# Performance work log

Hardware: AMD Instinct MI355X
Metric: run time of the kernel (lower is better)

Reference implementation:

```python
import jax, jax.numpy as jnp
import numpy as np

R = 0.4          # ball radius
K = 32           # max_neighbors
S = 512          # cluster_num
BN_EPS = 1e-5


def fps(data, npoint):
    """Furthest point sampling. data: [B,N,C] -> idx [B,npoint] int32.
    Deterministic start at index 0 (original uses randint)."""
    B, N, C = data.shape

    def step(carry, _):
        dist, far = carry
        cent = jnp.take_along_axis(data, far[:, None, None], axis=1)  # [B,1,C]
        d = jnp.sum((data - cent) ** 2, -1)                           # [B,N]
        dist = jnp.minimum(dist, d)
        new_far = jnp.argmax(dist, -1).astype(jnp.int32)
        return (dist, new_far), far

    dist0 = jnp.full((B, N), 1e10, data.dtype)
    far0 = jnp.zeros((B,), jnp.int32)
    _, idxs = jax.lax.scan(step, (dist0, far0), None, length=npoint)
    return idxs.T  # [B,npoint]


def gather_points(data, idx):
    """data [B,N,C], idx [B,S] -> [B,S,C]"""
    return jnp.take_along_axis(data, idx[..., None], axis=1)


def gather_groups(data, idx):
    """data [B,N,C], idx [B,S,K] -> [B,S,K,C]"""
    B, N, C = data.shape
    _, Sq, Kq = idx.shape
    flat = jnp.take_along_axis(data, idx.reshape(B, Sq * Kq)[..., None], axis=1)
    return flat.reshape(B, Sq, Kq, C)


def square_dist(a, b):
    """a [B,N,C], b [B,M,C] -> [B,N,M]"""
    return (-2.0 * jnp.einsum('bnc,bmc->bnm', a, b)
            + jnp.sum(a ** 2, -1)[:, :, None]
            + jnp.sum(b ** 2, -1)[:, None, :])


def knn_query(data, query, max_neighbors, r):
    """Ball query: indices of up to max_neighbors points within r, padded with
    the first valid index. data [B,N,C], query [B,S,C] -> [B,S,K] int32."""
    B, N, _ = data.shape
    d = square_dist(query, data)                              # [B,S,N]
    idx = jnp.where(d <= r * r, jnp.arange(N, dtype=jnp.int32)[None, None, :], N)
    idx = jnp.sort(idx, axis=-1)[:, :, :max_neighbors]        # ascending, N = invalid
    first = idx[:, :, :1]
    return jnp.where(idx == N, first, idx)


def mlp_layer(x, w, b, g, be):
    """1x1 Conv2d + BatchNorm2d (training-mode batch stats) + ReLU.
    x [B,S,K,Cin], w [Cout,Cin] -> [B,S,K,Cout]"""
    y = jnp.einsum('bskc,oc->bsko', x, w) + b
    m = jnp.mean(y, axis=(0, 1, 2))
    v = jnp.var(y, axis=(0, 1, 2))
    y = (y - m) * jax.lax.rsqrt(v + BN_EPS) * g + be
    return jax.nn.relu(y)


def setup_inputs() -> dict:
    key = jax.random.key(0)
    ks = jax.random.split(key, 5)
    B, N = 16, 8192
    data = jax.random.normal(ks[0], (B, N, 3), jnp.float32)
    data_feature = jax.random.normal(ks[1], (B, N, 3), jnp.float32)
    w0 = jax.random.normal(ks[2], (64, 6), jnp.float32) * 0.1
    w1 = jax.random.normal(ks[3], (64, 64), jnp.float32) * 0.1
    w2 = jax.random.normal(ks[4], (128, 64), jnp.float32) * 0.1
    zeros = lambda c: jnp.zeros((c,), jnp.float32)
    ones = lambda c: jnp.ones((c,), jnp.float32)
    return dict(data=data, data_feature=data_feature,
                w0=w0, b0=zeros(64), g0=ones(64), be0=zeros(64),
                w1=w1, b1=zeros(64), g1=ones(64), be1=zeros(64),
                w2=w2, b2=zeros(128), g2=ones(128), be2=zeros(128))


def reference(data, data_feature, w0, b0, g0, be0, w1, b1, g1, be1, w2, b2, g2, be2):
    B, N, C = data.shape
    fps_idx = fps(data, S)                              # [B,S]
    centroids = gather_points(data, fps_idx)            # [B,S,3]
    nbr_idx = knn_query(data, centroids, K, R)          # [B,S,K]
    sample = gather_groups(data, nbr_idx)               # [B,S,K,3]
    sample_norm = sample - centroids[:, :, None, :]
    feat = gather_groups(data_feature, nbr_idx)         # [B,S,K,3]
    x = jnp.concatenate([sample_norm, feat], axis=-1)   # [B,S,K,6]
    x = mlp_layer(x, w0, b0, g0, be0)
    x = mlp_layer(x, w1, b1, g1, be1)
    x = mlp_layer(x, w2, b2, g2, be2)
    out = jnp.max(x, axis=2)                            # [B,S,128]
    return centroids, out
```

## Files before the change

### kernel.cpp

```cpp
#include <hip/hip_runtime.h>
#include <math.h>

constexpr int Bc = 16;
constexpr int Nc = 8192;
constexpr int Sc = 512;
constexpr int Kc = 32;
constexpr int Pc = Bc * Sc * Kc;

constexpr int NBALL_BLK = 240;
constexpr int NBALL_WAVES = NBALL_BLK * 4;

typedef float v2f __attribute__((ext_vector_type(2)));

#if defined(__has_builtin)
#if __has_builtin(__builtin_elementwise_fma)
#define PKFMA(a, b, c) __builtin_elementwise_fma(a, b, c)
#endif
#endif
#ifndef PKFMA
__device__ __forceinline__ v2f pkfma_(v2f a, v2f b, v2f c) {
  v2f r; r.x = fmaf(a.x, b.x, c.x); r.y = fmaf(a.y, b.y, c.y); return r;
}
#define PKFMA(a, b, c) pkfma_(a, b, c)
#endif

template <int CTRL>
__device__ __forceinline__ float dpp_max_stage(float x) {
  int p = __builtin_amdgcn_update_dpp(0, __float_as_int(x), CTRL, 0xf, 0xf, true);
  return fmaxf(x, __int_as_float(p));
}

__global__ __launch_bounds__(256, 1)
void fps_ball_fused(const float* __restrict__ data,
                    const float* __restrict__ feat,
                    const float* __restrict__ w0,
                    const float* __restrict__ b0,
                    int* __restrict__ idx_pub,
                    float* __restrict__ cent_out,
                    float* __restrict__ x0,
                    float* __restrict__ part0) {
  __shared__ float lx[Nc], ly[Nc], lz[Nc];
  __shared__ unsigned long long red_k[2][4];
  __shared__ int idx_hist[Sc];
  __shared__ int nbr[4][Kc];
  __shared__ float x0s[4][6][Kc];

  const int t = threadIdx.x;
  const int lane = t & 63, w = t >> 6;

  if (blockIdx.x < Bc) {
    const int b = blockIdx.x;
    const float* db = data + (size_t)b * Nc * 3;

    float px[32], py[32], pz[32], dist[32];
#pragma unroll
    for (int j = 0; j < 32; ++j) {
      int p = t + 256 * j;
      px[j] = db[p * 3 + 0];
      py[j] = db[p * 3 + 1];
      pz[j] = db[p * 3 + 2];
      dist[j] = 1e10f;
      lx[p] = px[j]; ly[p] = py[j]; lz[p] = pz[j];
    }
    __syncthreads();

    int far = 0;
    for (int it = 0; it < Sc; ++it) {
      const int sfar = __builtin_amdgcn_readfirstlane(far);
      if (t == 0) {
        idx_hist[it] = sfar;
        atomicExch(&idx_pub[(b << 9) + it], sfar);
      }
      const float cx = lx[sfar];
      const float cy = ly[sfar];
      const float cz = lz[sfar];

      float best = -1.0f; int bj = 0;
#pragma unroll
      for (int j = 0; j < 32; ++j) {
        float dx = __fsub_rn(px[j], cx);
        float dy = __fsub_rn(py[j], cy);
        float dz = __fsub_rn(pz[j], cz);
        float d = __fadd_rn(__fadd_rn(__fmul_rn(dx, dx), __fmul_rn(dy, dy)),
                            __fmul_rn(dz, dz));
        float nd = fminf(dist[j], d);
        dist[j] = nd;
        if (nd > best) { best = nd; bj = j; }
      }
      const int bidx = t + 256 * bj;

      float wmax = best;
      wmax = dpp_max_stage<0xB1>(wmax);
      wmax = dpp_max_stage<0x4E>(wmax);
      wmax = dpp_max_stage<0x141>(wmax);
      wmax = dpp_max_stage<0x140>(wmax);
      wmax = fmaxf(wmax, __shfl_xor(wmax, 16));
      wmax = fmaxf(wmax, __shfl_xor(wmax, 32));

      unsigned long long m = __ballot(best == wmax);
      int idx;
      if (__popcll(m) == 1) {
        idx = __shfl(bidx, (int)__ffsll((long long)m) - 1);
      } else {
        int cand = (best == wmax) ? bidx : 0x7fffffff;
#pragma unroll
        for (int off = 32; off; off >>= 1) cand = min(cand, __shfl_xor(cand, off));
        idx = cand;
      }

      unsigned long long key =
          ((unsigned long long)__float_as_uint(wmax) << 32) |
          (unsigned long long)(0xFFFFFFFFu - (unsigned)idx);
      const int par = it & 1;
      if (lane == 0) red_k[par][w] = key;
      __syncthreads();

      unsigned long long k0 = red_k[par][0];
      unsigned long long k1 = red_k[par][1];
      unsigned long long k2 = red_k[par][2];
      unsigned long long k3 = red_k[par][3];
      unsigned long long ka = (k0 > k1) ? k0 : k1;
      unsigned long long kb = (k2 > k3) ? k2 : k3;
      unsigned long long kk = (ka > kb) ? ka : kb;
      far = (int)(0xFFFFFFFFu - (unsigned)(kk & 0xFFFFFFFFull));
    }

    __syncthreads();
    for (int s = t; s < Sc; s += 256) {
      int id = idx_hist[s];
      size_t o = ((size_t)b * Sc + s) * 3;
      cent_out[o + 0] = lx[id];
      cent_out[o + 1] = ly[id];
      cent_out[o + 2] = lz[id];
    }
  } else {
    const int wid = (blockIdx.x - Bc) * 4 + w;
    const int bb = wid & 15;
    const int u  = wid >> 4;
    const float* db = data + (size_t)bb * Nc * 3;
    const float* fb = feat + (size_t)bb * Nc * 3;

    float W[6];
#pragma unroll
    for (int c = 0; c < 6; ++c) W[c] = w0[lane * 6 + c];
    const float bias = b0[lane];
    float sum = 0.f, sq = 0.f;

    for (int s = u; s < Sc; s += 60) {
      const int q = bb * Sc + s;

      float px = db[lane * 3 + 0];
      float py = db[lane * 3 + 1];
      float pz = db[lane * 3 + 2];

      int ci;
      for (;;) {
        int t0 = -1;
        if (lane == 0) t0 = atomicAdd(&idx_pub[q], 0);
        ci = __shfl(t0, 0);
        if (ci >= 0) break;
        __builtin_amdgcn_s_sleep(32);
      }

      const float qx = db[ci * 3 + 0];
      const float qy = db[ci * 3 + 1];
      const float qz = db[ci * 3 + 2];
      const float q2 = __fadd_rn(__fadd_rn(__fmul_rn(qx, qx), __fmul_rn(qy, qy)),
                                 __fmul_rn(qz, qz));

      int have = 0;
      for (int base = 0; base < Nc; base += 64) {
        const int inext = (base + 64 + lane) & (Nc - 1);
        float nx = db[inext * 3 + 0];
        float ny = db[inext * 3 + 1];
        float nz = db[inext * 3 + 2];

        float p2 = __fadd_rn(__fadd_rn(__fmul_rn(px, px), __fmul_rn(py, py)),
                             __fmul_rn(pz, pz));
        float dt = fmaf(qz, pz, fmaf(qy, py, __fmul_rn(qx, px)));
        float d = __fadd_rn(__fadd_rn(__fmul_rn(-2.0f, dt), q2), p2);
        bool ok = d <= 0.16f;
        unsigned long long mask = __ballot(ok);
        if (mask) {
          int pos = have + __popcll(mask & ((1ull << lane) - 1ull));
          if (ok && pos < Kc) nbr[w][pos] = base + lane;
          have += __popcll(mask);
          if (have >= Kc) break;
        }
        px = nx; py = ny; pz = nz;
      }
      if (have > Kc) have = Kc;

      if (lane < Kc) {
        int j = nbr[w][lane < have ? lane : 0];
        float sx = __fsub_rn(db[j * 3 + 0], qx);
        float sy = __fsub_rn(db[j * 3 + 1], qy);
        float sz = __fsub_rn(db[j * 3 + 2], qz);
        float fx = fb[j * 3 + 0], fy = fb[j * 3 + 1], fz = fb[j * 3 + 2];
        size_t pidx = (size_t)q * Kc + lane;
        x0[(size_t)0 * Pc + pidx] = sx;
        x0[(size_t)1 * Pc + pidx] = sy;
        x0[(size_t)2 * Pc + pidx] = sz;
        x0[(size_t)3 * Pc + pidx] = fx;
        x0[(size_t)4 * Pc + pidx] = fy;
        x0[(size_t)5 * Pc + pidx] = fz;
        x0s[w][0][lane] = sx; x0s[w][1][lane] = sy; x0s[w][2][lane] = sz;
        x0s[w][3][lane] = fx; x0s[w][4][lane] = fy; x0s[w][5][lane] = fz;
      }

#pragma unroll 4
      for (int k = 0; k < Kc; ++k) {
        float y = bias;
#pragma unroll
        for (int c = 0; c < 6; ++c) y = fmaf(x0s[w][c][k], W[c], y);
        sum += y;
        sq = fmaf(y, y, sq);
      }
    }
    part0[(size_t)wid * 128 + lane] = sum;
    part0[(size_t)wid * 128 + 64 + lane] = sq;
  }
}

__global__ __launch_bounds__(256)
void reduce_k(const float* __restrict__ part, int nblk, int nch,
              const float* __restrict__ g, const float* __restrict__ be,
              float* __restrict__ AB) {
  const int o = blockIdx.x;
  const int t = threadIdx.x;
  double sum = 0.0, sq = 0.0;
  for (int i = t; i < nblk; i += 256) {
    sum += (double)part[(size_t)i * (2 * nch) + o];
    sq  += (double)part[(size_t)i * (2 * nch) + nch + o];
  }
  __shared__ double ls[256], lq[256];
  ls[t] = sum; lq[t] = sq;
  __syncthreads();
  for (int s = 128; s > 0; s >>= 1) {
    if (t < s) { ls[t] += ls[t + s]; lq[t] += lq[t + s]; }
    __syncthreads();
  }
  if (t == 0) {
    double m = ls[0] / (double)Pc;
    double v = lq[0] / (double)Pc - m * m;
    double A = (double)g[o] / sqrt(v + 1e-5);
    AB[o] = (float)A;
    AB[nch + o] = (float)((double)be[o] - m * A);
  }
}

__global__ __launch_bounds__(256)
void reduce2_final_k(const float* __restrict__ part, int nblk,
                     const float* __restrict__ g, const float* __restrict__ be,
                     const float* __restrict__ maxy2,
                     float* __restrict__ out) {
  const int o = blockIdx.x;
  const int t = threadIdx.x;
  double sum = 0.0, sq = 0.0;
  for (int i = t; i < nblk; i += 256) {
    sum += (double)part[(size_t)i * 256 + o];
    sq  += (double)part[(size_t)i * 256 + 128 + o];
  }
  __shared__ double ls[256], lq[256];
  ls[t] = sum; lq[t] = sq;
  __syncthreads();
  for (int s = 128; s > 0; s >>= 1) {
    if (t < s) { ls[t] += ls[t + s]; lq[t] += lq[t + s]; }
    __syncthreads();
  }
  __shared__ float sA, sB;
  if (t == 0) {
    double m = ls[0] / (double)Pc;
    double v = lq[0] / (double)Pc - m * m;
    double A = (double)g[o] / sqrt(v + 1e-5);
    sA = (float)A;
    sB = (float)((double)be[o] - m * A);
  }
  __syncthreads();
  const float A = sA, B = sB;
  for (int grp = t; grp < Bc * Sc; grp += 256) {
    float v = maxy2[(size_t)grp * 128 + o];
    out[(size_t)grp * 128 + o] = fmaxf(fmaf(v, A, B), 0.f);
  }
}

__global__ __launch_bounds__(256)
void pass_b(const float* __restrict__ x0, const float* __restrict__ w0,
            const float* __restrict__ b0, const float* __restrict__ AB0,
            const float* __restrict__ w1, const float* __restrict__ b1,
            float* __restrict__ y1, float* __restrict__ part1) {
  const int p = blockIdx.x * 256 + threadIdx.x;
  const int lane = threadIdx.x & 63, w = threadIdx.x >> 6;

  float xin[6];
#pragma unroll
  for (int c = 0; c < 6; ++c) xin[c] = x0[(size_t)c * Pc + p];

  float x1s[64];
#pragma unroll
  for (int o = 0; o < 64; ++o) {
    float y = b0[o];
#pragma unroll
    for (int c = 0; c < 6; ++c) y = fmaf(xin[c], w0[o * 6 + c], y);
    x1s[o] = fmaxf(fmaf(y, AB0[o], AB0[64 + o]), 0.f);
  }
  v2f x1p[32];
#pragma unroll
  for (int j = 0; j < 32; ++j) { x1p[j].x = x1s[2 * j]; x1p[j].y = x1s[2 * j + 1]; }

  const v2f* __restrict__ w1v = (const v2f*)w1;

  __shared__ float ssum[4][64][17], ssq[4][64][17];

  for (int o = 0; o < 64; ++o) {
    v2f a01; a01.x = b1[o]; a01.y = 0.f;
    v2f a23; a23.x = 0.f;   a23.y = 0.f;
#pragma unroll
    for (int c2 = 0; c2 < 32; c2 += 2) {
      a01 = PKFMA(x1p[c2 + 0], w1v[o * 32 + c2 + 0], a01);
      a23 = PKFMA(x1p[c2 + 1], w1v[o * 32 + c2 + 1], a23);
    }
    float acc = (a01.x + a01.y) + (a23.x + a23.y);
    y1[(size_t)o * Pc + p] = acc;

    float sv = acc + __shfl_xor(acc, 1);
    sv += __shfl_xor(sv, 2);
    float q = acc * acc;
    float qv = q + __shfl_xor(q, 1);
    qv += __shfl_xor(qv, 2);
    if ((lane & 3) == 0) {
      ssum[w][o][lane >> 2] = sv;
      ssq[w][o][lane >> 2] = qv;
    }
  }
  __syncthreads();
  if (threadIdx.x < 128) {
    const int o = threadIdx.x & 63;
    const bool isq = threadIdx.x >= 64;
    float s = 0.f;
#pragma unroll
    for (int ww = 0; ww < 4; ++ww)
      for (int k = 0; k < 16; ++k)
        s += isq ? ssq[ww][o][k] : ssum[ww][o][k];
    part1[blockIdx.x * 128 + threadIdx.x] = s;
  }
}

__global__ __launch_bounds__(256)
void pass_c(const float* __restrict__ y1, const float* __restrict__ AB1,
            const float* __restrict__ w2, const float* __restrict__ b2,
            float* __restrict__ maxy2, float* __restrict__ part2) {
  const int p = blockIdx.x * 256 + threadIdx.x;
  const int lane = threadIdx.x & 63, w = threadIdx.x >> 6;
  const int grp = p >> 5;

  v2f x2p[32];
#pragma unroll
  for (int c = 0; c < 64; c += 2) {
    float v0 = y1[(size_t)c * Pc + p];
    float v1 = y1[(size_t)(c + 1) * Pc + p];
    x2p[c >> 1].x = fmaxf(fmaf(v0, AB1[c], AB1[64 + c]), 0.f);
    x2p[c >> 1].y = fmaxf(fmaf(v1, AB1[c + 1], AB1[64 + c + 1]), 0.f);
  }

  const v2f* __restrict__ w2v = (const v2f*)w2;

  __shared__ float ssum[4][128][9], ssq[4][128][9];

  for (int o = 0; o < 128; ++o) {
    v2f a01; a01.x = b2[o]; a01.y = 0.f;
    v2f a23; a23.x = 0.f;   a23.y = 0.f;
#pragma unroll
    for (int c2 = 0; c2 < 32; c2 += 2) {
      a01 = PKFMA(x2p[c2 + 0], w2v[o * 32 + c2 + 0], a01);
      a23 = PKFMA(x2p[c2 + 1], w2v[o * 32 + c2 + 1], a23);
    }
    float acc = (a01.x + a01.y) + (a23.x + a23.y);

    float mx = acc;
#pragma unroll
    for (int off = 16; off > 0; off >>= 1) mx = fmaxf(mx, __shfl_xor(mx, off));
    if ((lane & 31) == 0) maxy2[(size_t)grp * 128 + o] = mx;

    float sv = acc + __shfl_xor(acc, 1);
    sv += __shfl_xor(sv, 2);
    sv += __shfl_xor(sv, 4);
    float q = acc * acc;
    float qv = q + __shfl_xor(q, 1);
    qv += __shfl_xor(qv, 2);
    qv += __shfl_xor(qv, 4);
    if ((lane & 7) == 0) {
      ssum[w][o][lane >> 3] = sv;
      ssq[w][o][lane >> 3] = qv;
    }
  }
  __syncthreads();
  {
    const int o = threadIdx.x & 127;
    const bool isq = threadIdx.x >= 128;
    float s = 0.f;
#pragma unroll
    for (int ww = 0; ww < 4; ++ww)
      for (int k = 0; k < 8; ++k)
        s += isq ? ssq[ww][o][k] : ssum[ww][o][k];
    part2[blockIdx.x * 256 + threadIdx.x] = s;
  }
}

extern "C" void kernel_launch(void* const* d_in, const int* in_sizes, int n_in,
                              void* d_out, int out_size, void* d_ws, size_t ws_size,
                              hipStream_t stream) {
  const float* data = (const float*)d_in[0];
  const float* feat = (const float*)d_in[1];
  const float* w0 = (const float*)d_in[2];
  const float* b0 = (const float*)d_in[3];
  const float* g0 = (const float*)d_in[4];
  const float* be0 = (const float*)d_in[5];
  const float* w1 = (const float*)d_in[6];
  const float* b1 = (const float*)d_in[7];
  const float* g1 = (const float*)d_in[8];
  const float* be1 = (const float*)d_in[9];
  const float* w2 = (const float*)d_in[10];
  const float* b2 = (const float*)d_in[11];
  const float* g2 = (const float*)d_in[12];
  const float* be2 = (const float*)d_in[13];
  float* out = (float*)d_out;

  float* ws = (float*)d_ws;
  int* idx_pub = (int*)ws; ws += (size_t)Bc * Sc;
  float* x0 = ws;      ws += (size_t)6 * Pc;
  float* y1 = ws;      ws += (size_t)64 * Pc;
  float* maxy2 = ws;   ws += (size_t)Bc * Sc * 128;
  float* part0 = ws;   ws += (size_t)NBALL_WAVES * 128;
  float* part1 = ws;   ws += 1024 * 128;
  float* part2 = ws;   ws += 1024 * 256;
  float* AB0 = ws;     ws += 128;
  float* AB1 = ws;     ws += 128;

  hipMemsetAsync(idx_pub, 0xFF, (size_t)Bc * Sc * sizeof(int), stream);

  fps_ball_fused<<<Bc + NBALL_BLK, 256, 0, stream>>>(data, feat, w0, b0,
                                                     idx_pub, out, x0, part0);
  reduce_k<<<64, 256, 0, stream>>>(part0, NBALL_WAVES, 64, g0, be0, AB0);
  pass_b<<<Pc / 256, 256, 0, stream>>>(x0, w0, b0, AB0, w1, b1, y1, part1);
  reduce_k<<<64, 256, 0, stream>>>(part1, 1024, 64, g1, be1, AB1);
  pass_c<<<Pc / 256, 256, 0, stream>>>(y1, AB1, w2, b2, maxy2, part2);
  reduce2_final_k<<<128, 256, 0, stream>>>(part2, 1024, g2, be2, maxy2,
                                           out + (size_t)Bc * Sc * 3);
}
```

Before: 793.3 us.

## Recompute layer-1 activations in pass_c instead of storing y1; shrink ball-query grid

pass_b no longer writes the 64-channel y1 intermediate, which is 64*Pc floats (about 67 MB). It only computes the BN statistics. pass_c recomputes layers 0 and 1 from x0 in registers before layer 2, trading a large global write and read for extra FMA work. The ball-query/layer-0 part of the fused kernel also drops from 240 to 60 blocks, with the stride adjusted to match, so each wave handles more centroids.

```diff
diff --git a/kernel.cpp b/kernel.cpp
--- a/kernel.cpp
+++ b/kernel.cpp
@@ -7,7 +7,7 @@
 constexpr int Kc = 32;
 constexpr int Pc = Bc * Sc * Kc;
 
-constexpr int NBALL_BLK = 240;
+constexpr int NBALL_BLK = 60;
 constexpr int NBALL_WAVES = NBALL_BLK * 4;
 
 typedef float v2f __attribute__((ext_vector_type(2)));
@@ -146,7 +146,7 @@
     const float bias = b0[lane];
     float sum = 0.f, sq = 0.f;
 
-    for (int s = u; s < Sc; s += 60) {
+    for (int s = u; s < Sc; s += 15) {
       const int q = bb * Sc + s;
 
       float px = db[lane * 3 + 0];
@@ -288,7 +288,7 @@
 void pass_b(const float* __restrict__ x0, const float* __restrict__ w0,
             const float* __restrict__ b0, const float* __restrict__ AB0,
             const float* __restrict__ w1, const float* __restrict__ b1,
-            float* __restrict__ y1, float* __restrict__ part1) {
+            float* __restrict__ part1) {
   const int p = blockIdx.x * 256 + threadIdx.x;
   const int lane = threadIdx.x & 63, w = threadIdx.x >> 6;
 
@@ -321,7 +321,6 @@
       a23 = PKFMA(x1p[c2 + 1], w1v[o * 32 + c2 + 1], a23);
     }
     float acc = (a01.x + a01.y) + (a23.x + a23.y);
-    y1[(size_t)o * Pc + p] = acc;
 
     float sv = acc + __shfl_xor(acc, 1);
     sv += __shfl_xor(sv, 2);
@@ -347,20 +346,55 @@
 }
 
 __global__ __launch_bounds__(256)
-void pass_c(const float* __restrict__ y1, const float* __restrict__ AB1,
+void pass_c(const float* __restrict__ x0, const float* __restrict__ w0,
+            const float* __restrict__ b0, const float* __restrict__ AB0,
+            const float* __restrict__ w1, const float* __restrict__ b1,
+            const float* __restrict__ AB1,
             const float* __restrict__ w2, const float* __restrict__ b2,
             float* __restrict__ maxy2, float* __restrict__ part2) {
   const int p = blockIdx.x * 256 + threadIdx.x;
   const int lane = threadIdx.x & 63, w = threadIdx.x >> 6;
   const int grp = p >> 5;
 
+  float xin[6];
+#pragma unroll
+  for (int c = 0; c < 6; ++c) xin[c] = x0[(size_t)c * Pc + p];
+
+  float x1s[64];
+#pragma unroll
+  for (int o = 0; o < 64; ++o) {
+    float y = b0[o];
+#pragma unroll
+    for (int c = 0; c < 6; ++c) y = fmaf(xin[c], w0[o * 6 + c], y);
+    x1s[o] = fmaxf(fmaf(y, AB0[o], AB0[64 + o]), 0.f);
+  }
+  v2f x1p[32];
+#pragma unroll
+  for (int j = 0; j < 32; ++j) { x1p[j].x = x1s[2 * j]; x1p[j].y = x1s[2 * j + 1]; }
+
+  const v2f* __restrict__ w1v = (const v2f*)w1;
+
   v2f x2p[32];
-#pragma unroll
-  for (int c = 0; c < 64; c += 2) {
-    float v0 = y1[(size_t)c * Pc + p];
-    float v1 = y1[(size_t)(c + 1) * Pc + p];
-    x2p[c >> 1].x = fmaxf(fmaf(v0, AB1[c], AB1[64 + c]), 0.f);
-    x2p[c >> 1].y = fmaxf(fmaf(v1, AB1[c + 1], AB1[64 + c + 1]), 0.f);
+  for (int o = 0; o < 64; o += 2) {
+    v2f a01; a01.x = b1[o]; a01.y = 0.f;
+    v2f a23; a23.x = 0.f;   a23.y = 0.f;
+#pragma unroll
+    for (int c2 = 0; c2 < 32; c2 += 2) {
+      a01 = PKFMA(x1p[c2 + 0], w1v[o * 32 + c2 + 0], a01);
+      a23 = PKFMA(x1p[c2 + 1], w1v[o * 32 + c2 + 1], a23);
+    }
+    float v0 = (a01.x + a01.y) + (a23.x + a23.y);
+    v2f b01; b01.x = b1[o + 1]; b01.y = 0.f;
+    v2f b23; b23.x = 0.f;       b23.y = 0.f;
+#pragma unroll
+    for (int c2 = 0; c2 < 32; c2 += 2) {
+      b01 = PKFMA(x1p[c2 + 0], w1v[(o + 1) * 32 + c2 + 0], b01);
+      b23 = PKFMA(x1p[c2 + 1], w1v[(o + 1) * 32 + c2 + 1], b23);
+    }
+    float v1 = (b01.x + b01.y) + (b23.x + b23.y);
+
+    x2p[o >> 1].x = fmaxf(fmaf(v0, AB1[o], AB1[64 + o]), 0.f);
+    x2p[o >> 1].y = fmaxf(fmaf(v1, AB1[o + 1], AB1[64 + o + 1]), 0.f);
   }
 
   const v2f* __restrict__ w2v = (const v2f*)w2;
@@ -429,7 +463,6 @@
   float* ws = (float*)d_ws;
   int* idx_pub = (int*)ws; ws += (size_t)Bc * Sc;
   float* x0 = ws;      ws += (size_t)6 * Pc;
-  float* y1 = ws;      ws += (size_t)64 * Pc;
   float* maxy2 = ws;   ws += (size_t)Bc * Sc * 128;
   float* part0 = ws;   ws += (size_t)NBALL_WAVES * 128;
   float* part1 = ws;   ws += 1024 * 128;
@@ -442,9 +475,10 @@
   fps_ball_fused<<<Bc + NBALL_BLK, 256, 0, stream>>>(data, feat, w0, b0,
                                                      idx_pub, out, x0, part0);
   reduce_k<<<64, 256, 0, stream>>>(part0, NBALL_WAVES, 64, g0, be0, AB0);
-  pass_b<<<Pc / 256, 256, 0, stream>>>(x0, w0, b0, AB0, w1, b1, y1, part1);
+  pass_b<<<Pc / 256, 256, 0, stream>>>(x0, w0, b0, AB0, w1, b1, part1);
   reduce_k<<<64, 256, 0, stream>>>(part1, 1024, 64, g1, be1, AB1);
-  pass_c<<<Pc / 256, 256, 0, stream>>>(y1, AB1, w2, b2, maxy2, part2);
+  pass_c<<<Pc / 256, 256, 0, stream>>>(x0, w0, b0, AB0, w1, b1, AB1,
+                                       w2, b2, maxy2, part2);
   reduce2_final_k<<<128, 256, 0, stream>>>(part2, 1024, g2, be2, maxy2,
                                            out + (size_t)Bc * Sc * 3);
 }
```

Result: slower. 1.169 ms (+47.4%).

## Fuse downstream MLP passes and BN reductions into one persistent kernel with grid barriers

Applied to the files above, without the earlier changes.

Replaces five separate launches (two reduce_k, pass_b, pass_c, reduce2_final_k) with a single persistent kernel of 512 blocks. Each block handles two 256-point tiles, and software grid barriers built on atomic counters separate the stages. The aim is to remove per-launch overhead and the tail gaps between the small reduction kernels. The barriers rely on all 512 blocks being co-resident, which is not guaranteed by the launch, so a deadlock is possible. Fewer blocks per stage also changes the work distribution.

```diff
diff --git a/kernel.cpp b/kernel.cpp
--- a/kernel.cpp
+++ b/kernel.cpp
@@ -9,6 +9,7 @@
 
 constexpr int NBALL_BLK = 240;
 constexpr int NBALL_WAVES = NBALL_BLK * 4;
+constexpr int DS_BLK = 512;
 
 typedef float v2f __attribute__((ext_vector_type(2)));
 
@@ -28,6 +29,17 @@
 __device__ __forceinline__ float dpp_max_stage(float x) {
   int p = __builtin_amdgcn_update_dpp(0, __float_as_int(x), CTRL, 0xf, 0xf, true);
   return fmaxf(x, __int_as_float(p));
+}
+
+__device__ __forceinline__ void grid_sync(int* ctr, int nblk) {
+  __syncthreads();
+  if (threadIdx.x == 0) {
+    __threadfence();
+    atomicAdd(ctr, 1);
+    while (atomicAdd(ctr, 0) < nblk) __builtin_amdgcn_s_sleep(4);
+    __threadfence();
+  }
+  __syncthreads();
 }
 
 __global__ __launch_bounds__(256, 1)
@@ -222,188 +234,227 @@
   }
 }
 
-__global__ __launch_bounds__(256)
-void reduce_k(const float* __restrict__ part, int nblk, int nch,
-              const float* __restrict__ g, const float* __restrict__ be,
-              float* __restrict__ AB) {
-  const int o = blockIdx.x;
+__global__ __launch_bounds__(256, 2)
+void downstream_mega(const float* __restrict__ x0,
+                     const float* __restrict__ w0, const float* __restrict__ b0,
+                     const float* __restrict__ w1, const float* __restrict__ b1,
+                     const float* __restrict__ w2, const float* __restrict__ b2,
+                     const float* __restrict__ g0, const float* __restrict__ be0,
+                     const float* __restrict__ g1, const float* __restrict__ be1,
+                     const float* __restrict__ g2, const float* __restrict__ be2,
+                     const float* __restrict__ part0,
+                     float* __restrict__ y1,
+                     float* __restrict__ part1, float* __restrict__ part2,
+                     float* __restrict__ maxy2,
+                     float* __restrict__ AB0, float* __restrict__ AB1,
+                     int* __restrict__ bars,
+                     float* __restrict__ out) {
+  const int g = blockIdx.x;
   const int t = threadIdx.x;
-  double sum = 0.0, sq = 0.0;
-  for (int i = t; i < nblk; i += 256) {
-    sum += (double)part[(size_t)i * (2 * nch) + o];
-    sq  += (double)part[(size_t)i * (2 * nch) + nch + o];
-  }
-  __shared__ double ls[256], lq[256];
-  ls[t] = sum; lq[t] = sq;
-  __syncthreads();
-  for (int s = 128; s > 0; s >>= 1) {
-    if (t < s) { ls[t] += ls[t + s]; lq[t] += lq[t + s]; }
-    __syncthreads();
-  }
-  if (t == 0) {
-    double m = ls[0] / (double)Pc;
-    double v = lq[0] / (double)Pc - m * m;
-    double A = (double)g[o] / sqrt(v + 1e-5);
-    AB[o] = (float)A;
-    AB[nch + o] = (float)((double)be[o] - m * A);
-  }
-}
-
-__global__ __launch_bounds__(256)
-void reduce2_final_k(const float* __restrict__ part, int nblk,
-                     const float* __restrict__ g, const float* __restrict__ be,
-                     const float* __restrict__ maxy2,
-                     float* __restrict__ out) {
-  const int o = blockIdx.x;
-  const int t = threadIdx.x;
-  double sum = 0.0, sq = 0.0;
-  for (int i = t; i < nblk; i += 256) {
-    sum += (double)part[(size_t)i * 256 + o];
-    sq  += (double)part[(size_t)i * 256 + 128 + o];
-  }
-  __shared__ double ls[256], lq[256];
-  ls[t] = sum; lq[t] = sq;
-  __syncthreads();
-  for (int s = 128; s > 0; s >>= 1) {
-    if (t < s) { ls[t] += ls[t + s]; lq[t] += lq[t + s]; }
-    __syncthreads();
-  }
-  __shared__ float sA, sB;
-  if (t == 0) {
-    double m = ls[0] / (double)Pc;
-    double v = lq[0] / (double)Pc - m * m;
-    double A = (double)g[o] / sqrt(v + 1e-5);
-    sA = (float)A;
-    sB = (float)((double)be[o] - m * A);
-  }
-  __syncthreads();
-  const float A = sA, B = sB;
-  for (int grp = t; grp < Bc * Sc; grp += 256) {
-    float v = maxy2[(size_t)grp * 128 + o];
-    out[(size_t)grp * 128 + o] = fmaxf(fmaf(v, A, B), 0.f);
-  }
-}
-
-__global__ __launch_bounds__(256)
-void pass_b(const float* __restrict__ x0, const float* __restrict__ w0,
-            const float* __restrict__ b0, const float* __restrict__ AB0,
-            const float* __restrict__ w1, const float* __restrict__ b1,
-            float* __restrict__ y1, float* __restrict__ part1) {
-  const int p = blockIdx.x * 256 + threadIdx.x;
-  const int lane = threadIdx.x & 63, w = threadIdx.x >> 6;
-
-  float xin[6];
-#pragma unroll
-  for (int c = 0; c < 6; ++c) xin[c] = x0[(size_t)c * Pc + p];
-
-  float x1s[64];
-#pragma unroll
-  for (int o = 0; o < 64; ++o) {
-    float y = b0[o];
-#pragma unroll
-    for (int c = 0; c < 6; ++c) y = fmaf(xin[c], w0[o * 6 + c], y);
-    x1s[o] = fmaxf(fmaf(y, AB0[o], AB0[64 + o]), 0.f);
-  }
-  v2f x1p[32];
-#pragma unroll
-  for (int j = 0; j < 32; ++j) { x1p[j].x = x1s[2 * j]; x1p[j].y = x1s[2 * j + 1]; }
-
-  const v2f* __restrict__ w1v = (const v2f*)w1;
-
-  __shared__ float ssum[4][64][17], ssq[4][64][17];
-
-  for (int o = 0; o < 64; ++o) {
-    v2f a01; a01.x = b1[o]; a01.y = 0.f;
-    v2f a23; a23.x = 0.f;   a23.y = 0.f;
-#pragma unroll
-    for (int c2 = 0; c2 < 32; c2 += 2) {
-      a01 = PKFMA(x1p[c2 + 0], w1v[o * 32 + c2 + 0], a01);
-      a23 = PKFMA(x1p[c2 + 1], w1v[o * 32 + c2 + 1], a23);
-    }
-    float acc = (a01.x + a01.y) + (a23.x + a23.y);
-    y1[(size_t)o * Pc + p] = acc;
-
-    float sv = acc + __shfl_xor(acc, 1);
-    sv += __shfl_xor(sv, 2);
-    float q = acc * acc;
-    float qv = q + __shfl_xor(q, 1);
-    qv += __shfl_xor(qv, 2);
-    if ((lane & 3) == 0) {
-      ssum[w][o][lane >> 2] = sv;
-      ssq[w][o][lane >> 2] = qv;
-    }
-  }
-  __syncthreads();
-  if (threadIdx.x < 128) {
-    const int o = threadIdx.x & 63;
-    const bool isq = threadIdx.x >= 64;
-    float s = 0.f;
-#pragma unroll
-    for (int ww = 0; ww < 4; ++ww)
-      for (int k = 0; k < 16; ++k)
-        s += isq ? ssq[ww][o][k] : ssum[ww][o][k];
-    part1[blockIdx.x * 128 + threadIdx.x] = s;
-  }
-}
-
-__global__ __launch_bounds__(256)
-void pass_c(const float* __restrict__ y1, const float* __restrict__ AB1,
-            const float* __restrict__ w2, const float* __restrict__ b2,
-            float* __restrict__ maxy2, float* __restrict__ part2) {
-  const int p = blockIdx.x * 256 + threadIdx.x;
-  const int lane = threadIdx.x & 63, w = threadIdx.x >> 6;
-  const int grp = p >> 5;
-
-  v2f x2p[32];
-#pragma unroll
-  for (int c = 0; c < 64; c += 2) {
-    float v0 = y1[(size_t)c * Pc + p];
-    float v1 = y1[(size_t)(c + 1) * Pc + p];
-    x2p[c >> 1].x = fmaxf(fmaf(v0, AB1[c], AB1[64 + c]), 0.f);
-    x2p[c >> 1].y = fmaxf(fmaf(v1, AB1[c + 1], AB1[64 + c + 1]), 0.f);
-  }
-
-  const v2f* __restrict__ w2v = (const v2f*)w2;
-
-  __shared__ float ssum[4][128][9], ssq[4][128][9];
-
-  for (int o = 0; o < 128; ++o) {
-    v2f a01; a01.x = b2[o]; a01.y = 0.f;
-    v2f a23; a23.x = 0.f;   a23.y = 0.f;
-#pragma unroll
-    for (int c2 = 0; c2 < 32; c2 += 2) {
-      a01 = PKFMA(x2p[c2 + 0], w2v[o * 32 + c2 + 0], a01);
-      a23 = PKFMA(x2p[c2 + 1], w2v[o * 32 + c2 + 1], a23);
-    }
-    float acc = (a01.x + a01.y) + (a23.x + a23.y);
-
-    float mx = acc;
-#pragma unroll
-    for (int off = 16; off > 0; off >>= 1) mx = fmaxf(mx, __shfl_xor(mx, off));
-    if ((lane & 31) == 0) maxy2[(size_t)grp * 128 + o] = mx;
-
-    float sv = acc + __shfl_xor(acc, 1);
-    sv += __shfl_xor(sv, 2);
-    sv += __shfl_xor(sv, 4);
-    float q = acc * acc;
-    float qv = q + __shfl_xor(q, 1);
-    qv += __shfl_xor(qv, 2);
-    qv += __shfl_xor(qv, 4);
-    if ((lane & 7) == 0) {
-      ssum[w][o][lane >> 3] = sv;
-      ssq[w][o][lane >> 3] = qv;
-    }
-  }
-  __syncthreads();
+  const int lane = t & 63, w = t >> 6;
+
+  __shared__ __align__(16) char smem[36864];
+
+  if (g < 64) {
+    double sum = 0.0, sq = 0.0;
+    for (int i = t; i < NBALL_WAVES; i += 256) {
+      sum += (double)part0[(size_t)i * 128 + g];
+      sq  += (double)part0[(size_t)i * 128 + 64 + g];
+    }
+    double* ls = (double*)smem;
+    double* lq = ls + 256;
+    ls[t] = sum; lq[t] = sq;
+    __syncthreads();
+    for (int s = 128; s > 0; s >>= 1) {
+      if (t < s) { ls[t] += ls[t + s]; lq[t] += lq[t + s]; }
+      __syncthreads();
+    }
+    if (t == 0) {
+      double m = ls[0] / (double)Pc;
+      double v = lq[0] / (double)Pc - m * m;
+      double A = (double)g0[g] / sqrt(v + 1e-5);
+      AB0[g] = (float)A;
+      AB0[64 + g] = (float)((double)be0[g] - m * A);
+    }
+  }
+  grid_sync(&bars[0], DS_BLK);
+
   {
-    const int o = threadIdx.x & 127;
-    const bool isq = threadIdx.x >= 128;
-    float s = 0.f;
-#pragma unroll
-    for (int ww = 0; ww < 4; ++ww)
-      for (int k = 0; k < 8; ++k)
-        s += isq ? ssq[ww][o][k] : ssum[ww][o][k];
-    part2[blockIdx.x * 256 + threadIdx.x] = s;
+    float (*ssum)[64][17] = (float (*)[64][17])smem;
+    float (*ssq )[64][17] = (float (*)[64][17])(smem + 4 * 64 * 17 * 4);
+    for (int i = t; i < 2 * 4 * 64 * 17; i += 256) ((float*)smem)[i] = 0.f;
+    __syncthreads();
+
+    const v2f* __restrict__ w1v = (const v2f*)w1;
+    for (int r = 0; r < 2; ++r) {
+      const int p = g * 512 + r * 256 + t;
+
+      float xin[6];
+#pragma unroll
+      for (int c = 0; c < 6; ++c) xin[c] = x0[(size_t)c * Pc + p];
+
+      float x1s[64];
+#pragma unroll
+      for (int o = 0; o < 64; ++o) {
+        float y = b0[o];
+#pragma unroll
+        for (int c = 0; c < 6; ++c) y = fmaf(xin[c], w0[o * 6 + c], y);
+        x1s[o] = fmaxf(fmaf(y, AB0[o], AB0[64 + o]), 0.f);
+      }
+      v2f x1p[32];
+#pragma unroll
+      for (int j = 0; j < 32; ++j) { x1p[j].x = x1s[2 * j]; x1p[j].y = x1s[2 * j + 1]; }
+
+      for (int o = 0; o < 64; ++o) {
+        v2f a01; a01.x = b1[o]; a01.y = 0.f;
+        v2f a23; a23.x = 0.f;   a23.y = 0.f;
+#pragma unroll
+        for (int c2 = 0; c2 < 32; c2 += 2) {
+          a01 = PKFMA(x1p[c2 + 0], w1v[o * 32 + c2 + 0], a01);
+          a23 = PKFMA(x1p[c2 + 1], w1v[o * 32 + c2 + 1], a23);
+        }
+        float acc = (a01.x + a01.y) + (a23.x + a23.y);
+        y1[(size_t)o * Pc + p] = acc;
+
+        float sv = acc + __shfl_xor(acc, 1);
+        sv += __shfl_xor(sv, 2);
+        float q = acc * acc;
+        float qv = q + __shfl_xor(q, 1);
+        qv += __shfl_xor(qv, 2);
+        if ((lane & 3) == 0) {
+          ssum[w][o][lane >> 2] += sv;
+          ssq[w][o][lane >> 2] += qv;
+        }
+      }
+    }
+    __syncthreads();
+    if (t < 128) {
+      const int o = t & 63;
+      const bool isq = t >= 64;
+      float s = 0.f;
+#pragma unroll
+      for (int ww = 0; ww < 4; ++ww)
+        for (int k = 0; k < 16; ++k)
+          s += isq ? ssq[ww][o][k] : ssum[ww][o][k];
+      part1[(size_t)g * 128 + t] = s;
+    }
+  }
+  grid_sync(&bars[1], DS_BLK);
+
+  if (g < 64) {
+    double sum = 0.0, sq = 0.0;
+    for (int i = t; i < DS_BLK; i += 256) {
+      sum += (double)part1[(size_t)i * 128 + g];
+      sq  += (double)part1[(size_t)i * 128 + 64 + g];
+    }
+    double* ls = (double*)smem;
+    double* lq = ls + 256;
+    ls[t] = sum; lq[t] = sq;
+    __syncthreads();
+    for (int s = 128; s > 0; s >>= 1) {
+      if (t < s) { ls[t] += ls[t + s]; lq[t] += lq[t + s]; }
+      __syncthreads();
+    }
+    if (t == 0) {
+      double m = ls[0] / (double)Pc;
+      double v = lq[0] / (double)Pc - m * m;
+      double A = (double)g1[g] / sqrt(v + 1e-5);
+      AB1[g] = (float)A;
+      AB1[64 + g] = (float)((double)be1[g] - m * A);
+    }
+  }
+  grid_sync(&bars[2], DS_BLK);
+
+  {
+    float (*ssum)[128][9] = (float (*)[128][9])smem;
+    float (*ssq )[128][9] = (float (*)[128][9])(smem + 4 * 128 * 9 * 4);
+    for (int i = t; i < 2 * 4 * 128 * 9; i += 256) ((float*)smem)[i] = 0.f;
+    __syncthreads();
+
+    const v2f* __restrict__ w2v = (const v2f*)w2;
+    for (int r = 0; r < 2; ++r) {
+      const int p = g * 512 + r * 256 + t;
+      const int grp = p >> 5;
+
+      v2f x2p[32];
+#pragma unroll
+      for (int c = 0; c < 64; c += 2) {
+        float v0 = y1[(size_t)c * Pc + p];
+        float v1 = y1[(size_t)(c + 1) * Pc + p];
+        x2p[c >> 1].x = fmaxf(fmaf(v0, AB1[c], AB1[64 + c]), 0.f);
+        x2p[c >> 1].y = fmaxf(fmaf(v1, AB1[c + 1], AB1[64 + c + 1]), 0.f);
+      }
+
+      for (int o = 0; o < 128; ++o) {
+        v2f a01; a01.x = b2[o]; a01.y = 0.f;
+        v2f a23; a23.x = 0.f;   a23.y = 0.f;
+#pragma unroll
+        for (int c2 = 0; c2 < 32; c2 += 2) {
+          a01 = PKFMA(x2p[c2 + 0], w2v[o * 32 + c2 + 0], a01);
+          a23 = PKFMA(x2p[c2 + 1], w2v[o * 32 + c2 + 1], a23);
+        }
+        float acc = (a01.x + a01.y) + (a23.x + a23.y);
+
+        float mx = acc;
+#pragma unroll
+        for (int off = 16; off > 0; off >>= 1) mx = fmaxf(mx, __shfl_xor(mx, off));
+        if ((lane & 31) == 0) maxy2[(size_t)grp * 128 + o] = mx;
+
+        float sv = acc + __shfl_xor(acc, 1);
+        sv += __shfl_xor(sv, 2);
+        sv += __shfl_xor(sv, 4);
+        float q = acc * acc;
+        float qv = q + __shfl_xor(q, 1);
+        qv += __shfl_xor(qv, 2);
+        qv += __shfl_xor(qv, 4);
+        if ((lane & 7) == 0) {
+          ssum[w][o][lane >> 3] += sv;
+          ssq[w][o][lane >> 3] += qv;
+        }
+      }
+    }
+    __syncthreads();
+    {
+      const int o = t & 127;
+      const bool isq = t >= 128;
+      float s = 0.f;
+#pragma unroll
+      for (int ww = 0; ww < 4; ++ww)
+        for (int k = 0; k < 8; ++k)
+          s += isq ? ssq[ww][o][k] : ssum[ww][o][k];
+      part2[(size_t)g * 256 + t] = s;
+    }
+  }
+  grid_sync(&bars[3], DS_BLK);
+
+  if (g < 128) {
+    double sum = 0.0, sq = 0.0;
+    for (int i = t; i < DS_BLK; i += 256) {
+      sum += (double)part2[(size_t)i * 256 + g];
+      sq  += (double)part2[(size_t)i * 256 + 128 + g];
+    }
+    double* ls = (double*)smem;
+    double* lq = ls + 256;
+    ls[t] = sum; lq[t] = sq;
+    __syncthreads();
+    for (int s = 128; s > 0; s >>= 1) {
+      if (t < s) { ls[t] += ls[t + s]; lq[t] += lq[t + s]; }
+      __syncthreads();
+    }
+    float* sAB = (float*)(smem + 4096);
+    if (t == 0) {
+      double m = ls[0] / (double)Pc;
+      double v = lq[0] / (double)Pc - m * m;
+      double A = (double)g2[g] / sqrt(v + 1e-5);
+      sAB[0] = (float)A;
+      sAB[1] = (float)((double)be2[g] - m * A);
+    }
+    __syncthreads();
+    const float A = sAB[0], B = sAB[1];
+    for (int grp = t; grp < Bc * Sc; grp += 256) {
+      float v = maxy2[(size_t)grp * 128 + g];
+      out[(size_t)grp * 128 + g] = fmaxf(fmaf(v, A, B), 0.f);
+    }
   }
 }
 
@@ -428,23 +479,23 @@
 
   float* ws = (float*)d_ws;
   int* idx_pub = (int*)ws; ws += (size_t)Bc * Sc;
+  int* bars = (int*)ws;    ws += 8;
   float* x0 = ws;      ws += (size_t)6 * Pc;
   float* y1 = ws;      ws += (size_t)64 * Pc;
   float* maxy2 = ws;   ws += (size_t)Bc * Sc * 128;
   float* part0 = ws;   ws += (size_t)NBALL_WAVES * 128;
-  float* part1 = ws;   ws += 1024 * 128;
-  float* part2 = ws;   ws += 1024 * 256;
+  float* part1 = ws;   ws += (size_t)DS_BLK * 128;
+  float* part2 = ws;   ws += (size_t)DS_BLK * 256;
   float* AB0 = ws;     ws += 128;
   float* AB1 = ws;     ws += 128;
 
   hipMemsetAsync(idx_pub, 0xFF, (size_t)Bc * Sc * sizeof(int), stream);
+  hipMemsetAsync(bars, 0, 8 * sizeof(int), stream);
 
   fps_ball_fused<<<Bc + NBALL_BLK, 256, 0, stream>>>(data, feat, w0, b0,
                                                      idx_pub, out, x0, part0);
-  reduce_k<<<64, 256, 0, stream>>>(part0, NBALL_WAVES, 64, g0, be0, AB0);
-  pass_b<<<Pc / 256, 256, 0, stream>>>(x0, w0, b0, AB0, w1, b1, y1, part1);
-  reduce_k<<<64, 256, 0, stream>>>(part1, 1024, 64, g1, be1, AB1);
-  pass_c<<<Pc / 256, 256, 0, stream>>>(y1, AB1, w2, b2, maxy2, part2);
-  reduce2_final_k<<<128, 256, 0, stream>>>(part2, 1024, g2, be2, maxy2,
-                                           out + (size_t)Bc * Sc * 3);
+  downstream_mega<<<DS_BLK, 256, 0, stream>>>(
+      x0, w0, b0, w1, b1, w2, b2, g0, be0, g1, be1, g2, be2,
+      part0, y1, part1, part2, maxy2, AB0, AB1, bars,
+      out + (size_t)Bc * Sc * 3);
 }
```

Result: slower. 1.113 ms (+40.2%).

## Remap MLP passes to lane-per-output-channel with register weights and LDS activations

Applied to the files above, without the earlier changes.

Rewrites pass_b and pass_c so each lane owns one output channel, holding its weight row in registers. Point activations are staged in LDS and read as broadcast float4 vectors. The y1 intermediate becomes point-major for coalesced stores and loads. Per-output shuffle reductions for max and batch-norm statistics are replaced by per-lane running accumulators, and the partial-sum buffers grow to match. This costs more registers per thread and extra LDS traffic and syncs.

```diff
diff --git a/kernel.cpp b/kernel.cpp
--- a/kernel.cpp
+++ b/kernel.cpp
@@ -289,122 +289,115 @@
             const float* __restrict__ b0, const float* __restrict__ AB0,
             const float* __restrict__ w1, const float* __restrict__ b1,
             float* __restrict__ y1, float* __restrict__ part1) {
-  const int p = blockIdx.x * 256 + threadIdx.x;
-  const int lane = threadIdx.x & 63, w = threadIdx.x >> 6;
-
-  float xin[6];
-#pragma unroll
-  for (int c = 0; c < 6; ++c) xin[c] = x0[(size_t)c * Pc + p];
-
-  float x1s[64];
-#pragma unroll
-  for (int o = 0; o < 64; ++o) {
-    float y = b0[o];
-#pragma unroll
-    for (int c = 0; c < 6; ++c) y = fmaf(xin[c], w0[o * 6 + c], y);
-    x1s[o] = fmaxf(fmaf(y, AB0[o], AB0[64 + o]), 0.f);
-  }
-  v2f x1p[32];
-#pragma unroll
-  for (int j = 0; j < 32; ++j) { x1p[j].x = x1s[2 * j]; x1p[j].y = x1s[2 * j + 1]; }
-
-  const v2f* __restrict__ w1v = (const v2f*)w1;
-
-  __shared__ float ssum[4][64][17], ssq[4][64][17];
-
-  for (int o = 0; o < 64; ++o) {
-    v2f a01; a01.x = b1[o]; a01.y = 0.f;
-    v2f a23; a23.x = 0.f;   a23.y = 0.f;
-#pragma unroll
-    for (int c2 = 0; c2 < 32; c2 += 2) {
-      a01 = PKFMA(x1p[c2 + 0], w1v[o * 32 + c2 + 0], a01);
-      a23 = PKFMA(x1p[c2 + 1], w1v[o * 32 + c2 + 1], a23);
-    }
-    float acc = (a01.x + a01.y) + (a23.x + a23.y);
-    y1[(size_t)o * Pc + p] = acc;
-
-    float sv = acc + __shfl_xor(acc, 1);
-    sv += __shfl_xor(sv, 2);
-    float q = acc * acc;
-    float qv = q + __shfl_xor(q, 1);
-    qv += __shfl_xor(qv, 2);
-    if ((lane & 3) == 0) {
-      ssum[w][o][lane >> 2] = sv;
-      ssq[w][o][lane >> 2] = qv;
-    }
-  }
-  __syncthreads();
-  if (threadIdx.x < 128) {
-    const int o = threadIdx.x & 63;
-    const bool isq = threadIdx.x >= 64;
-    float s = 0.f;
-#pragma unroll
-    for (int ww = 0; ww < 4; ++ww)
-      for (int k = 0; k < 16; ++k)
-        s += isq ? ssq[ww][o][k] : ssum[ww][o][k];
-    part1[blockIdx.x * 128 + threadIdx.x] = s;
-  }
+  const int t = threadIdx.x;
+  const int lane = t & 63, w = t >> 6;
+  const int wid = blockIdx.x * 4 + w;
+  const int base = wid * 64;
+
+  __shared__ float x0s[4][6][32];
+  __shared__ float x1t[4][32][64];
+
+  float W0[6];
+#pragma unroll
+  for (int c = 0; c < 6; ++c) W0[c] = w0[lane * 6 + c];
+  const float B0 = b0[lane];
+  const float A0 = AB0[lane], C0 = AB0[64 + lane];
+  v2f W1[32];
+#pragma unroll
+  for (int j = 0; j < 32; ++j) W1[j] = ((const v2f*)w1)[lane * 32 + j];
+  const float B1 = b1[lane];
+
+  float sum = 0.f, sq = 0.f;
+
+  for (int ch = 0; ch < 2; ++ch) {
+    const int pb = base + ch * 32;
+#pragma unroll
+    for (int r = 0; r < 3; ++r) {
+      int c = r * 2 + (lane >> 5);
+      int pt = lane & 31;
+      x0s[w][c][pt] = x0[(size_t)c * Pc + pb + pt];
+    }
+    for (int pt = 0; pt < 32; ++pt) {
+      float y = B0;
+#pragma unroll
+      for (int c = 0; c < 6; ++c) y = fmaf(x0s[w][c][pt], W0[c], y);
+      x1t[w][pt][lane] = fmaxf(fmaf(y, A0, C0), 0.f);
+    }
+    for (int pt = 0; pt < 32; ++pt) {
+      const float4* xr = (const float4*)&x1t[w][pt][0];
+      v2f a01; a01.x = B1; a01.y = 0.f;
+      v2f a23; a23.x = 0.f; a23.y = 0.f;
+#pragma unroll
+      for (int kk = 0; kk < 16; ++kk) {
+        float4 f = xr[kk];
+        v2f lo; lo.x = f.x; lo.y = f.y;
+        v2f hi; hi.x = f.z; hi.y = f.w;
+        a01 = PKFMA(lo, W1[2 * kk + 0], a01);
+        a23 = PKFMA(hi, W1[2 * kk + 1], a23);
+      }
+      float acc = (a01.x + a01.y) + (a23.x + a23.y);
+      y1[(size_t)(pb + pt) * 64 + lane] = acc;
+      sum += acc;
+      sq = fmaf(acc, acc, sq);
+    }
+  }
+  part1[(size_t)wid * 128 + lane] = sum;
+  part1[(size_t)wid * 128 + 64 + lane] = sq;
 }
 
 __global__ __launch_bounds__(256)
 void pass_c(const float* __restrict__ y1, const float* __restrict__ AB1,
             const float* __restrict__ w2, const float* __restrict__ b2,
             float* __restrict__ maxy2, float* __restrict__ part2) {
-  const int p = blockIdx.x * 256 + threadIdx.x;
-  const int lane = threadIdx.x & 63, w = threadIdx.x >> 6;
-  const int grp = p >> 5;
-
-  v2f x2p[32];
-#pragma unroll
-  for (int c = 0; c < 64; c += 2) {
-    float v0 = y1[(size_t)c * Pc + p];
-    float v1 = y1[(size_t)(c + 1) * Pc + p];
-    x2p[c >> 1].x = fmaxf(fmaf(v0, AB1[c], AB1[64 + c]), 0.f);
-    x2p[c >> 1].y = fmaxf(fmaf(v1, AB1[c + 1], AB1[64 + c + 1]), 0.f);
-  }
-
-  const v2f* __restrict__ w2v = (const v2f*)w2;
-
-  __shared__ float ssum[4][128][9], ssq[4][128][9];
-
-  for (int o = 0; o < 128; ++o) {
-    v2f a01; a01.x = b2[o]; a01.y = 0.f;
-    v2f a23; a23.x = 0.f;   a23.y = 0.f;
-#pragma unroll
-    for (int c2 = 0; c2 < 32; c2 += 2) {
-      a01 = PKFMA(x2p[c2 + 0], w2v[o * 32 + c2 + 0], a01);
-      a23 = PKFMA(x2p[c2 + 1], w2v[o * 32 + c2 + 1], a23);
-    }
-    float acc = (a01.x + a01.y) + (a23.x + a23.y);
-
-    float mx = acc;
-#pragma unroll
-    for (int off = 16; off > 0; off >>= 1) mx = fmaxf(mx, __shfl_xor(mx, off));
-    if ((lane & 31) == 0) maxy2[(size_t)grp * 128 + o] = mx;
-
-    float sv = acc + __shfl_xor(acc, 1);
-    sv += __shfl_xor(sv, 2);
-    sv += __shfl_xor(sv, 4);
-    float q = acc * acc;
-    float qv = q + __shfl_xor(q, 1);
-    qv += __shfl_xor(qv, 2);
-    qv += __shfl_xor(qv, 4);
-    if ((lane & 7) == 0) {
-      ssum[w][o][lane >> 3] = sv;
-      ssq[w][o][lane >> 3] = qv;
-    }
-  }
-  __syncthreads();
-  {
-    const int o = threadIdx.x & 127;
-    const bool isq = threadIdx.x >= 128;
-    float s = 0.f;
-#pragma unroll
-    for (int ww = 0; ww < 4; ++ww)
-      for (int k = 0; k < 8; ++k)
-        s += isq ? ssq[ww][o][k] : ssum[ww][o][k];
-    part2[blockIdx.x * 256 + threadIdx.x] = s;
-  }
+  const int t = threadIdx.x;
+  const int lane = t & 63, w = t >> 6;
+  const int pr = w >> 1;
+  const int h = w & 1;
+  const int o = h * 64 + lane;
+  const int pair = blockIdx.x * 2 + pr;
+  const int base = pair * 128;
+
+  __shared__ float x2t[2][32][64];
+
+  const float A1 = AB1[lane], C1 = AB1[64 + lane];
+  v2f W2[32];
+#pragma unroll
+  for (int j = 0; j < 32; ++j) W2[j] = ((const v2f*)w2)[o * 32 + j];
+  const float B2 = b2[o];
+
+  float sum = 0.f, sq = 0.f;
+
+  for (int ch = 0; ch < 4; ++ch) {
+    const int pb = base + ch * 32;
+    __syncthreads();
+    for (int i = 0; i < 16; ++i) {
+      int pt = h * 16 + i;
+      float v = y1[(size_t)(pb + pt) * 64 + lane];
+      x2t[pr][pt][lane] = fmaxf(fmaf(v, A1, C1), 0.f);
+    }
+    __syncthreads();
+    float mx = 0.f;
+    for (int pt = 0; pt < 32; ++pt) {
+      const float4* xr = (const float4*)&x2t[pr][pt][0];
+      v2f a01; a01.x = B2; a01.y = 0.f;
+      v2f a23; a23.x = 0.f; a23.y = 0.f;
+#pragma unroll
+      for (int kk = 0; kk < 16; ++kk) {
+        float4 f = xr[kk];
+        v2f lo; lo.x = f.x; lo.y = f.y;
+        v2f hi; hi.x = f.z; hi.y = f.w;
+        a01 = PKFMA(lo, W2[2 * kk + 0], a01);
+        a23 = PKFMA(hi, W2[2 * kk + 1], a23);
+      }
+      float acc = (a01.x + a01.y) + (a23.x + a23.y);
+      mx = (pt == 0) ? acc : fmaxf(mx, acc);
+      sum += acc;
+      sq = fmaf(acc, acc, sq);
+    }
+    maxy2[(size_t)(pb >> 5) * 128 + o] = mx;
+  }
+  part2[(size_t)pair * 256 + o] = sum;
+  part2[(size_t)pair * 256 + 128 + o] = sq;
 }
 
 extern "C" void kernel_launch(void* const* d_in, const int* in_sizes, int n_in,
@@ -432,8 +425,8 @@
   float* y1 = ws;      ws += (size_t)64 * Pc;
   float* maxy2 = ws;   ws += (size_t)Bc * Sc * 128;
   float* part0 = ws;   ws += (size_t)NBALL_WAVES * 128;
-  float* part1 = ws;   ws += 1024 * 128;
-  float* part2 = ws;   ws += 1024 * 256;
+  float* part1 = ws;   ws += (size_t)4096 * 128;
+  float* part2 = ws;   ws += (size_t)2048 * 256;
   float* AB0 = ws;     ws += 128;
   float* AB1 = ws;     ws += 128;
 
@@ -442,9 +435,9 @@
   fps_ball_fused<<<Bc + NBALL_BLK, 256, 0, stream>>>(data, feat, w0, b0,
                                                      idx_pub, out, x0, part0);
   reduce_k<<<64, 256, 0, stream>>>(part0, NBALL_WAVES, 64, g0, be0, AB0);
-  pass_b<<<Pc / 256, 256, 0, stream>>>(x0, w0, b0, AB0, w1, b1, y1, part1);
-  reduce_k<<<64, 256, 0, stream>>>(part1, 1024, 64, g1, be1, AB1);
-  pass_c<<<Pc / 256, 256, 0, stream>>>(y1, AB1, w2, b2, maxy2, part2);
-  reduce2_final_k<<<128, 256, 0, stream>>>(part2, 1024, g2, be2, maxy2,
+  pass_b<<<1024, 256, 0, stream>>>(x0, w0, b0, AB0, w1, b1, y1, part1);
+  reduce_k<<<64, 256, 0, stream>>>(part1, 4096, 64, g1, be1, AB1);
+  pass_c<<<1024, 256, 0, stream>>>(y1, AB1, w2, b2, maxy2, part2);
+  reduce2_final_k<<<128, 256, 0, stream>>>(part2, 2048, g2, be2, maxy2,
                                            out + (size_t)Bc * Sc * 3);
 }
```

New measurement: 805.5 us. No clear change (+1.5%).
